# Kernel optimization log

Measured on AMD Instinct MI355X. Metric: run time of the kernel, lower is better.

Reference implementation:

```python
import jax, jax.numpy as jnp
import numpy as np

VOCAB, D_MODEL, HEADS, PAD_ID = 32000, 512, 8, 0
D_K = D_MODEL // HEADS
EPS = 1e-5


def pos_encoding(T, d):
    pos = jnp.arange(T, dtype=jnp.float32)[:, None]              # [T,1]
    freqs = 1.0 / (10000.0 ** (jnp.arange(0, d, 2, dtype=jnp.float32) / d))
    ang = pos * freqs                                            # [T,d/2]
    pe = jnp.zeros((T, d), dtype=jnp.float32)
    pe = pe.at[:, 0::2].set(jnp.sin(ang)).at[:, 1::2].set(jnp.cos(ang))
    return pe


def layer_norm(x, g, b):
    mu = jnp.mean(x, axis=-1, keepdims=True)
    var = jnp.var(x, axis=-1, keepdims=True)
    return (x - mu) * jax.lax.rsqrt(var + EPS) * g + b


def setup_inputs() -> dict:
    key = jax.random.key(0)
    ks = jax.random.split(key, 12)
    B, T = 4, 2048
    s = 0.02
    inp = {
        "tokens": jax.random.randint(ks[0], (B, T), 0, VOCAB),
        "emb": jax.random.normal(ks[1], (VOCAB, D_MODEL), jnp.float32) * s,
        "wq": jax.random.normal(ks[2], (D_MODEL, D_MODEL), jnp.float32) * s,
        "bq": jnp.zeros((D_MODEL,), jnp.float32),
        "wk": jax.random.normal(ks[3], (D_MODEL, D_MODEL), jnp.float32) * s,
        "bk": jnp.zeros((D_MODEL,), jnp.float32),
        "wv": jax.random.normal(ks[4], (D_MODEL, D_MODEL), jnp.float32) * s,
        "bv": jnp.zeros((D_MODEL,), jnp.float32),
        "wo": jax.random.normal(ks[5], (D_MODEL, D_MODEL), jnp.float32) * s,
        "bo": jnp.zeros((D_MODEL,), jnp.float32),
        "w1": jax.random.normal(ks[6], (D_MODEL, 2 * D_MODEL), jnp.float32) * s,
        "b1": jnp.zeros((2 * D_MODEL,), jnp.float32),
        "w2": jax.random.normal(ks[7], (2 * D_MODEL, D_MODEL), jnp.float32) * s,
        "b2": jnp.zeros((D_MODEL,), jnp.float32),
        "ln1_g": jnp.ones((D_MODEL,), jnp.float32),
        "ln1_b": jnp.zeros((D_MODEL,), jnp.float32),
        "ln2_g": jnp.ones((D_MODEL,), jnp.float32),
        "ln2_b": jnp.zeros((D_MODEL,), jnp.float32),
    }
    return inp


def reference(tokens, emb, wq, bq, wk, bk, wv, bv, wo, bo,
              w1, b1, w2, b2, ln1_g, ln1_b, ln2_g, ln2_b):
    B, T = tokens.shape
    x = emb[tokens] * jnp.sqrt(jnp.float32(D_MODEL))             # [B,T,D]
    x = x + pos_encoding(T, D_MODEL)[None]                       # add PE
    q = (x @ wq + bq).reshape(B, T, HEADS, D_K)
    k = (x @ wk + bk).reshape(B, T, HEADS, D_K)
    v = (x @ wv + bv).reshape(B, T, HEADS, D_K)
    scores = jnp.einsum("bqhd,bkhd->bhqk", q, k) / jnp.sqrt(jnp.float32(D_K))
    key_pad_mask = tokens == PAD_ID                              # [B,T]
    neg = jnp.finfo(scores.dtype).min
    scores = jnp.where(key_pad_mask[:, None, None, :], neg, scores)
    attn = jax.nn.softmax(scores, axis=-1)                       # [B,H,T,T]
    av = jnp.einsum("bhqk,bkhd->bqhd", attn, v).reshape(B, T, D_MODEL)
    av = av @ wo + bo
    h = layer_norm(av + x, ln1_g, ln1_b)
    ff = jax.nn.relu(h @ w1 + b1) @ w2 + b2
    out = layer_norm(h + ff, ln2_g, ln2_b)
    return out, key_pad_mask
```

## Files before the change

kernel.cpp:

```cpp
#include <hip/hip_runtime.h>
#include <hip/hip_bf16.h>
#include <math.h>

#define D_MODEL 512
#define HEADS   8
#define D_K     64
#define T_SEQ   2048
#define B_SZ    4
#define NROWS   (B_SZ * T_SEQ)
#define KVB     64
#define KSPLIT  2
#define KHALF   (T_SEQ / KSPLIT)

#define BN 128
#define BKG 64

typedef __attribute__((ext_vector_type(8))) short short8;
typedef __attribute__((ext_vector_type(4))) float f32x4;
typedef __attribute__((ext_vector_type(4))) ushort bf16x4;
typedef __attribute__((ext_vector_type(4))) unsigned int u32x4;

typedef __attribute__((address_space(1))) const unsigned int as1_uint;
typedef __attribute__((address_space(3))) unsigned int as3_uint;

__device__ __forceinline__ ushort f2bf(float f) {
    union { float f; unsigned u; } v; v.f = f;
    unsigned u = v.u;
    unsigned r = (u + 0x7FFFu + ((u >> 16) & 1u)) >> 16;
    return (ushort)r;
}
__device__ __forceinline__ float bf2f(ushort u) {
    union { unsigned u; float f; } v; v.u = ((unsigned)u) << 16;
    return v.f;
}
__device__ __forceinline__ unsigned pk_bf16(float lo, float hi) {
    unsigned r;
    asm("v_cvt_pk_bf16_f32 %0, %1, %2" : "=v"(r) : "v"(lo), "v"(hi));
    return r;
}

__global__ __launch_bounds__(256) void k_prep(
    const int* __restrict__ tokens, const float* __restrict__ emb,
    const float* __restrict__ wq, const float* __restrict__ wk,
    const float* __restrict__ wv, const float* __restrict__ wo,
    const float* __restrict__ w1, const float* __restrict__ w2,
    const float* __restrict__ bq, const float* __restrict__ bk,
    const float* __restrict__ bv,
    ushort* __restrict__ xb, float* __restrict__ mask_out,
    ushort* __restrict__ wqkvT, ushort* __restrict__ woT,
    ushort* __restrict__ w1T, ushort* __restrict__ w2T,
    float* __restrict__ bqkv, float qsc)
{
    __shared__ ushort tls[32][33];
    int bid = blockIdx.x, tid = threadIdx.x;
    if (bid < 4096) {
        int row = bid * 2 + (tid >> 7);
        int t   = row & (T_SEQ - 1);
        int tok = tokens[row];
        int t2  = tid & 127;
        if (t2 == 0) mask_out[row] = (tok == 0) ? 1.0f : 0.0f;
        const float* e = emb + (size_t)tok * D_MODEL;
#pragma unroll
        for (int i = 0; i < 4; ++i) {
            int d = t2 + 128 * i;
            float freq = exp2f(-(float)(d & ~1) * 0.025952563240330564f);
            float sn, cs;
            sincosf((float)t * freq, &sn, &cs);
            float x = e[d] * 22.627416997969522f + ((d & 1) ? cs : sn);
            xb[(size_t)row * D_MODEL + d] = f2bf(x);
        }
        return;
    }
    const float* src; ushort* dst; float scale = 1.0f; int K, N, bx, by;
    if (bid < 5120) {
        int b = bid - 4096; int z = b >> 8; int rem = b & 255;
        bx = rem & 15; by = rem >> 4; K = 512; N = 512;
        src = (z == 0) ? wq : (z == 1) ? wk : (z == 2) ? wv : wo;
        dst = (z < 3) ? wqkvT + (size_t)z * 512 * 512 : woT;
        scale = (z == 0) ? qsc : 1.0f;
    } else if (bid < 5632) {
        int b = bid - 5120; bx = b & 31; by = b >> 5; K = 512; N = 1024; src = w1; dst = w1T;
    } else if (bid < 6144) {
        int b = bid - 5632; bx = b & 15; by = b >> 4; K = 1024; N = 512; src = w2; dst = w2T;
    } else {
        int i = (bid - 6144) * 256 + tid;
        if (i < 512)       bqkv[i] = bq[i] * qsc;
        else if (i < 1024) bqkv[i] = bk[i - 512];
        else if (i < 1536) bqkv[i] = bv[i - 1024];
        return;
    }
    int tx = tid & 31, ty = tid >> 5;
    int n0 = bx * 32, k0 = by * 32;
#pragma unroll
    for (int i = 0; i < 4; ++i)
        tls[ty + i * 8][tx] = f2bf(src[(size_t)(k0 + ty + i * 8) * N + n0 + tx] * scale);
    __syncthreads();
#pragma unroll
    for (int i = 0; i < 4; ++i)
        dst[(size_t)(n0 + ty + i * 8) * K + k0 + tx] = tls[tx][ty + i * 8];
}

__global__ __launch_bounds__(256) void k_rl(const float* __restrict__ lp,
                                            float* __restrict__ rl) {
    int i = blockIdx.x * 256 + threadIdx.x;
    rl[i] = 1.0f / (lp[i] + lp[8 * NROWS + i]);
}

template<int MODE, bool RELU, int BMT, bool COMBA>
__global__ __launch_bounds__(256) void k_gemm_lds(
    const ushort* __restrict__ A, const ushort* __restrict__ A2,
    const float* __restrict__ rlb,
    const ushort* __restrict__ BT,
    const float* __restrict__ bias, void* __restrict__ C0,
    void* __restrict__ C1, void* __restrict__ C2,
    int M, int N, int K)
{
    constexpr int MR = BMT / 32;
    __shared__ __attribute__((aligned(16))) ushort As[2][BMT * BKG];
    __shared__ __attribute__((aligned(16))) ushort Bs[2][BN * BKG];

    const int tid = threadIdx.x;
    const int w = tid >> 6, l = tid & 63;
    const int lr = l & 15, lg = l >> 4;
    const int wr = w >> 1, wc = w & 1;

    int bx = blockIdx.x, by = blockIdx.y;
    {
        int nx = gridDim.x, ny = gridDim.y;
        if ((ny & 7) == 0) {
            int lin = bx + nx * by;
            int xcd = lin & 7, idx = lin >> 3;
            int per = ny >> 3;
            by = xcd * per + (idx % per);
            bx = idx / per;
        }
    }
    const int brow0 = by * BMT;
    const int bcol0 = bx * BN;
    const int swz = lr & 7;

    f32x4 acc[MR][4] = {};
    const int nks = K >> 6;

#define STAGE_B(buf, k0)                                                        \
    {                                                                           \
        _Pragma("unroll")                                                       \
        for (int i = 0; i < 4; ++i) {                                           \
            int gi = w * 256 + i * 64 + l;                                      \
            int row = gi >> 3, slot = gi & 7;                                   \
            int g = slot ^ (row & 7);                                           \
            __builtin_amdgcn_global_load_lds(                                   \
                (as1_uint*)(BT + (size_t)(bcol0 + row) * K + (k0) + g * 8),     \
                (as3_uint*)(&Bs[buf][gi * 8]), 16, 0, 0);                       \
        }                                                                       \
    }
#define STAGE_A_DMA(buf, k0)                                                    \
    {                                                                           \
        _Pragma("unroll")                                                       \
        for (int i = 0; i < BMT / 32; ++i) {                                    \
            int gi = w * (BMT * 2) + i * 64 + l;                                \
            int row = gi >> 3, slot = gi & 7;                                   \
            int g = slot ^ (row & 7);                                           \
            __builtin_amdgcn_global_load_lds(                                   \
                (as1_uint*)(A + (size_t)(brow0 + row) * K + (k0) + g * 8),      \
                (as3_uint*)(&As[buf][gi * 8]), 16, 0, 0);                       \
        }                                                                       \
    }
#define STAGE_A_COMB(buf, k0)                                                   \
    {                                                                           \
        int head = (k0) >> 6;                                                   \
        _Pragma("unroll")                                                       \
        for (int i = 0; i < BMT / 32; ++i) {                                    \
            int gi = w * (BMT * 2) + i * 64 + l;                                \
            int row = gi >> 3, slot = gi & 7;                                   \
            int g = slot ^ (row & 7);                                           \
            size_t off = (size_t)(brow0 + row) * K + (k0) + g * 8;              \
            bf16x4 a0 = *(const bf16x4*)(A + off);                              \
            bf16x4 a1 = *(const bf16x4*)(A + off + 4);                          \
            bf16x4 c0 = *(const bf16x4*)(A2 + off);                             \
            bf16x4 c1 = *(const bf16x4*)(A2 + off + 4);                         \
            float r = rlb[(size_t)head * NROWS + brow0 + row];                  \
            u32x4 pk;                                                           \
            pk[0] = pk_bf16((bf2f(a0[0]) + bf2f(c0[0])) * r,                    \
                            (bf2f(a0[1]) + bf2f(c0[1])) * r);                   \
            pk[1] = pk_bf16((bf2f(a0[2]) + bf2f(c0[2])) * r,                    \
                            (bf2f(a0[3]) + bf2f(c0[3])) * r);                   \
            pk[2] = pk_bf16((bf2f(a1[0]) + bf2f(c1[0])) * r,                    \
                            (bf2f(a1[1]) + bf2f(c1[1])) * r);                   \
            pk[3] = pk_bf16((bf2f(a1[2]) + bf2f(c1[2])) * r,                    \
                            (bf2f(a1[3]) + bf2f(c1[3])) * r);                   \
            *(u32x4*)(&As[buf][gi * 8]) = pk;                                   \
        }                                                                       \
    }
#define STAGE(buf, k0)                                                          \
    {                                                                           \
        if constexpr (COMBA) { STAGE_A_COMB(buf, k0); }                         \
        else                 { STAGE_A_DMA(buf, k0); }                          \
        STAGE_B(buf, k0);                                                       \
    }

    STAGE(0, 0);
    __syncthreads();

    int buf = 0;
    for (int ks = 0; ks < nks; ++ks) {
        if (ks + 1 < nks) STAGE(buf ^ 1, (ks + 1) * BKG);
#pragma unroll
        for (int kk = 0; kk < 2; ++kk) {
            short8 af[MR], bfr[4];
#pragma unroll
            for (int m = 0; m < MR; ++m) {
                int row = wr * (BMT / 2) + m * 16 + lr;
                int slot = (kk * 4 + lg) ^ swz;
                af[m] = *(const short8*)(&As[buf][row * 64 + slot * 8]);
            }
#pragma unroll
            for (int n = 0; n < 4; ++n) {
                int row = wc * 64 + n * 16 + lr;
                int slot = (kk * 4 + lg) ^ swz;
                bfr[n] = *(const short8*)(&Bs[buf][row * 64 + slot * 8]);
            }
#pragma unroll
            for (int m = 0; m < MR; ++m)
#pragma unroll
                for (int n = 0; n < 4; ++n)
                    acc[m][n] = __builtin_amdgcn_mfma_f32_16x16x32_bf16(af[m], bfr[n], acc[m][n], 0, 0, 0);
        }
        __syncthreads();
        buf ^= 1;
    }
#undef STAGE
#undef STAGE_A_COMB
#undef STAGE_A_DMA
#undef STAGE_B

#pragma unroll
    for (int n = 0; n < 4; ++n) {
        int col = bcol0 + wc * 64 + n * 16 + lr;
        float bv = bias[col];
#pragma unroll
        for (int m = 0; m < MR; ++m) {
            int row0 = brow0 + wr * (BMT / 2) + m * 16 + 4 * lg;
            if constexpr (MODE == 2) {
                int seg = col >> 9, lc = col & 511;
                if (seg == 2) {
                    bf16x4 pk;
#pragma unroll
                    for (int j = 0; j < 4; ++j) pk[j] = f2bf(acc[m][n][j] + bv);
                    *(bf16x4*)((ushort*)C2 + (size_t)lc * M + row0) = pk;
                } else {
                    ushort* dst = (seg == 0) ? (ushort*)C0 : (ushort*)C1;
#pragma unroll
                    for (int j = 0; j < 4; ++j)
                        dst[(size_t)(row0 + j) * 512 + lc] = f2bf(acc[m][n][j] + bv);
                }
            } else if constexpr (MODE == 0) {
#pragma unroll
                for (int j = 0; j < 4; ++j) {
                    float v = acc[m][n][j] + bv;
                    if (RELU) v = fmaxf(v, 0.0f);
                    ((ushort*)C0)[(size_t)(row0 + j) * N + col] = f2bf(v);
                }
            } else {
#pragma unroll
                for (int j = 0; j < 4; ++j)
                    ((float*)C0)[(size_t)(row0 + j) * N + col] = acc[m][n][j] + bv;
            }
        }
    }
}

__global__ __launch_bounds__(512, 4) void k_attn(
    const ushort* __restrict__ Q, const ushort* __restrict__ Kb,
    const ushort* __restrict__ Vt, const int* __restrict__ tokens,
    ushort* __restrict__ O0, ushort* __restrict__ O1,
    float* __restrict__ lp)
{
    __shared__ __attribute__((aligned(16))) ushort Kl[2][KVB * 64];
    __shared__ __attribute__((aligned(16))) ushort Vl[2][KVB * 64];
    __shared__ __attribute__((aligned(16))) ushort Mbh[KHALF];
    __shared__ int padf[KHALF / KVB];

    const int tid = threadIdx.x;
    const int w = tid >> 6, l = tid & 63;
    const int lr = l & 15, lg = l >> 4;
    const int swz = lr & 7;

    int lin = blockIdx.x + 8 * (blockIdx.y + 8 * blockIdx.z);
    int xcd = lin & 7, idx = lin >> 3;
    int qt  = idx & 7;
    int grp = xcd + 8 * (idx >> 3);
    int ks  = grp & 1;
    int h   = (grp >> 1) & 7;
    int b   = grp >> 4;

    const int q0  = qt * 256 + w * 32;
    const int kb0 = ks * KHALF;

    const int gi   = w * 64 + l;
    const int srow = gi >> 3;
    const int sg   = gi & 7;
    const int sgx  = sg ^ (srow & 7);
    const ushort* Ksrc = Kb + ((size_t)(b * T_SEQ + kb0) + srow) * D_MODEL + h * D_K + sgx * 8;
    const int kbase = 32 * (sg >> 2) + 8 * ((sg >> 1) & 1) + 4 * (sg & 1);
    const ushort* Vsrc = Vt + (size_t)(h * D_K + srow) * NROWS + b * T_SEQ + kb0 + kbase;
    const int vds = srow * 128 + sgx * 16;

#define KSTAGE(bufi, kt_)                                                       \
    __builtin_amdgcn_global_load_lds(                                           \
        (as1_uint*)(Ksrc + (size_t)(kt_) * KVB * D_MODEL),                      \
        (as3_uint*)(&Kl[bufi][gi * 8]), 16, 0, 0);

    const ushort* Qh = Q + (size_t)b * T_SEQ * D_MODEL + h * D_K;
    short8 aq[2][2];
#pragma unroll
    for (int qs = 0; qs < 2; ++qs)
#pragma unroll
        for (int c2 = 0; c2 < 2; ++c2)
            aq[qs][c2] = *(const short8*)(Qh + (size_t)(q0 + qs * 16 + lr) * D_MODEL
                                          + c2 * 32 + 8 * lg);

    short8 vones;
#pragma unroll
    for (int i = 0; i < 8; ++i) vones[i] = (short)0x3F80;

    const int* tk = tokens + b * T_SEQ + kb0;
#pragma unroll
    for (int it = 0; it < KHALF / 512; ++it) {
        int i = tid + it * 512;
        bool pad = (tk[i] == 0);
        Mbh[i] = pad ? (ushort)0xFF7F : (ushort)0;
        unsigned long long bal = __ballot(pad);
        if (l == 0) padf[it * 8 + w] = (bal != 0ull);
    }

    f32x4 acc[2][4] = {};
    f32x4 acc_l[2] = {};

    {
        bf16x4 va = *(const bf16x4*)(Vsrc);
        bf16x4 vb2 = *(const bf16x4*)(Vsrc + 16);
        KSTAGE(0, 0);
        u32x4 pk = { ((const unsigned*)&va)[0], ((const unsigned*)&va)[1],
                     ((const unsigned*)&vb2)[0], ((const unsigned*)&vb2)[1] };
        *(u32x4*)((char*)Vl[0] + vds) = pk;
    }
    __syncthreads();

    int buf = 0;
    const int NT = KHALF / KVB;
#pragma unroll 2
    for (int kt = 0; kt < NT; ++kt) {
        bf16x4 vna, vnb;
        bool more = (kt + 1 < NT);
        if (more) {
            KSTAGE(buf ^ 1, kt + 1);
            vna = *(const bf16x4*)(Vsrc + (kt + 1) * KVB);
            vnb = *(const bf16x4*)(Vsrc + (kt + 1) * KVB + 16);
        }

        const ushort* Kt = Kl[buf];
        const ushort* Vb = Vl[buf];
        bool havePad = padf[kt];

        unsigned dw[2][4][2];
#pragma unroll
        for (int kh = 0; kh < 2; ++kh) {
            short8 kf[2][2];
#pragma unroll
            for (int i = 0; i < 2; ++i)
#pragma unroll
                for (int c2 = 0; c2 < 2; ++c2)
                    kf[i][c2] = *(const short8*)((const char*)Kt
                                + ((2 * kh + i) * 16 + lr) * 128
                                + (((c2 * 4 + lg) ^ swz) * 16));
#pragma unroll
            for (int qs = 0; qs < 2; ++qs)
#pragma unroll
                for (int i = 0; i < 2; ++i) {
                    int kb = 2 * kh + i;
                    __builtin_amdgcn_s_setprio(1);
                    f32x4 sf = {};
                    sf = __builtin_amdgcn_mfma_f32_16x16x32_bf16(kf[i][0], aq[qs][0], sf, 0, 0, 0);
                    sf = __builtin_amdgcn_mfma_f32_16x16x32_bf16(kf[i][1], aq[qs][1], sf, 0, 0, 0);
                    __builtin_amdgcn_s_setprio(0);
                    if (havePad) {
                        bf16x4 m4 = *(const bf16x4*)(Mbh + kt * KVB + kb * 16 + 4 * lg);
#pragma unroll
                        for (int j = 0; j < 4; ++j) sf[j] += bf2f(m4[j]);
                    }
                    dw[qs][kb][0] = pk_bf16(exp2f(sf[0]), exp2f(sf[1]));
                    dw[qs][kb][1] = pk_bf16(exp2f(sf[2]), exp2f(sf[3]));
                }
        }

#pragma unroll
        for (int ch = 0; ch < 2; ++ch) {
            short8 vf[2][2];
#pragma unroll
            for (int i = 0; i < 2; ++i)
#pragma unroll
                for (int kk = 0; kk < 2; ++kk)
                    vf[i][kk] = *(const short8*)((const char*)Vb
                                + ((2 * ch + i) * 16 + lr) * 128
                                + (((kk * 4 + lg) ^ swz) * 16));
            __builtin_amdgcn_s_setprio(1);
#pragma unroll
            for (int qs = 0; qs < 2; ++qs) {
                u32x4 pw0 = { dw[qs][0][0], dw[qs][0][1], dw[qs][1][0], dw[qs][1][1] };
                u32x4 pw1 = { dw[qs][2][0], dw[qs][2][1], dw[qs][3][0], dw[qs][3][1] };
                short8 pa0 = __builtin_bit_cast(short8, pw0);
                short8 pa1 = __builtin_bit_cast(short8, pw1);
#pragma unroll
                for (int i = 0; i < 2; ++i) {
                    int c = 2 * ch + i;
                    acc[qs][c] = __builtin_amdgcn_mfma_f32_16x16x32_bf16(vf[i][0], pa0, acc[qs][c], 0, 0, 0);
                    acc[qs][c] = __builtin_amdgcn_mfma_f32_16x16x32_bf16(vf[i][1], pa1, acc[qs][c], 0, 0, 0);
                }
                if (ch == 0) {
                    acc_l[qs] = __builtin_amdgcn_mfma_f32_16x16x32_bf16(vones, pa0, acc_l[qs], 0, 0, 0);
                    acc_l[qs] = __builtin_amdgcn_mfma_f32_16x16x32_bf16(vones, pa1, acc_l[qs], 0, 0, 0);
                }
            }
            __builtin_amdgcn_s_setprio(0);
        }

        if (more) {
            u32x4 pk = { ((const unsigned*)&vna)[0], ((const unsigned*)&vna)[1],
                         ((const unsigned*)&vnb)[0], ((const unsigned*)&vnb)[1] };
            *(u32x4*)((char*)Vl[buf ^ 1] + vds) = pk;
        }
        __syncthreads();
        buf ^= 1;
    }
#undef KSTAGE

    ushort* Op = (ks == 0) ? O0 : O1;
#pragma unroll
    for (int qs = 0; qs < 2; ++qs) {
        ushort* orow = Op + (size_t)(b * T_SEQ + q0 + qs * 16 + lr) * D_MODEL + h * D_K;
#pragma unroll
        for (int c = 0; c < 4; ++c) {
            bf16x4 pk;
#pragma unroll
            for (int j = 0; j < 4; ++j) pk[j] = f2bf(acc[qs][c][j]);
            *(bf16x4*)(orow + c * 16 + 4 * lg) = pk;
        }
        if (l < 16)
            lp[(size_t)(ks * 8 + h) * NROWS + b * T_SEQ + q0 + qs * 16 + l] = acc_l[qs][0];
    }
}

template<bool A_BF16, bool RES_BF16, bool OUT_F32>
__global__ __launch_bounds__(256) void k_ln(
    const void* __restrict__ A, const void* __restrict__ Res,
    const float* __restrict__ g, const float* __restrict__ bb,
    float* __restrict__ of, ushort* __restrict__ ob)
{
    int row = blockIdx.x * 4 + (threadIdx.x >> 6);
    int l = threadIdx.x & 63;
    float v[8];
    float s = 0.0f, ss = 0.0f;
#pragma unroll
    for (int i = 0; i < 2; ++i) {
        int d0 = i * 256 + l * 4;
        f32x4 va, vb;
        if (A_BF16) {
            bf16x4 t = *(const bf16x4*)((const ushort*)A + (size_t)row * D_MODEL + d0);
#pragma unroll
            for (int j = 0; j < 4; ++j) va[j] = bf2f(t[j]);
        } else {
            va = *(const f32x4*)((const float*)A + (size_t)row * D_MODEL + d0);
        }
        if (RES_BF16) {
            bf16x4 t = *(const bf16x4*)((const ushort*)Res + (size_t)row * D_MODEL + d0);
#pragma unroll
            for (int j = 0; j < 4; ++j) vb[j] = bf2f(t[j]);
        } else {
            vb = *(const f32x4*)((const float*)Res + (size_t)row * D_MODEL + d0);
        }
#pragma unroll
        for (int j = 0; j < 4; ++j) {
            float x = va[j] + vb[j];
            v[i * 4 + j] = x; s += x; ss += x * x;
        }
    }
#pragma unroll
    for (int d = 1; d < 64; d <<= 1) { s += __shfl_xor(s, d); ss += __shfl_xor(ss, d); }
    float mu  = s * (1.0f / 512.0f);
    float var = ss * (1.0f / 512.0f) - mu * mu;
    float rs  = rsqrtf(var + 1e-5f);
#pragma unroll
    for (int i = 0; i < 2; ++i)
#pragma unroll
        for (int j = 0; j < 4; ++j) {
            int d = i * 256 + l * 4 + j;
            float o = (v[i * 4 + j] - mu) * rs * g[d] + bb[d];
            if (OUT_F32) of[(size_t)row * D_MODEL + d] = o;
            else         ob[(size_t)row * D_MODEL + d] = f2bf(o);
        }
}

extern "C" void kernel_launch(void* const* d_in, const int* in_sizes, int n_in,
                              void* d_out, int out_size, void* d_ws, size_t ws_size,
                              hipStream_t stream)
{
    const int*   tokens = (const int*)  d_in[0];
    const float* emb    = (const float*)d_in[1];
    const float* wq     = (const float*)d_in[2];
    const float* bq     = (const float*)d_in[3];
    const float* wk     = (const float*)d_in[4];
    const float* bk     = (const float*)d_in[5];
    const float* wv     = (const float*)d_in[6];
    const float* bv     = (const float*)d_in[7];
    const float* wo     = (const float*)d_in[8];
    const float* bo     = (const float*)d_in[9];
    const float* w1     = (const float*)d_in[10];
    const float* b1     = (const float*)d_in[11];
    const float* w2     = (const float*)d_in[12];
    const float* b2     = (const float*)d_in[13];
    const float* ln1_g  = (const float*)d_in[14];
    const float* ln1_b  = (const float*)d_in[15];
    const float* ln2_g  = (const float*)d_in[16];
    const float* ln2_b  = (const float*)d_in[17];

    char* ws = (char*)d_ws;
    ushort* xb   = (ushort*)(ws + 0);
    ushort* Qb   = (ushort*)(ws + 8388608);
    ushort* Kbuf = (ushort*)(ws + 16777216);
    ushort* Vt   = (ushort*)(ws + 25165824);
    ushort* atb  = (ushort*)(ws + 33554432);
    ushort* AVb  = (ushort*)(ws + 41943040);
    ushort* wqkvT = (ushort*)(ws + 50331648);
    ushort* woT  = wqkvT + 1536 * 512;
    ushort* w1T  = woT + 262144;
    ushort* w2T  = w1T + 524288;
    float*  bqkv = (float*)(w2T + 524288);
    float*  lpart = bqkv + 2048;
    float*  rlbuf = lpart + 2 * 8 * NROWS;
    float*  WOf   = (float*)(rlbuf + 8 * NROWS);

    ushort* hb   = Qb;
    ushort* ff1b = Kbuf;
    ushort* ff2b = AVb;
    ushort* wob  = AVb;
    (void)WOf;

    float* out_f    = (float*)d_out;
    float* mask_out = out_f + (size_t)NROWS * D_MODEL;

    const float QSC = 0.18033688011112042f;

    k_prep<<<6150, 256, 0, stream>>>(
        tokens, emb, wq, wk, wv, wo, w1, w2, bq, bk, bv,
        xb, mask_out, wqkvT, woT, w1T, w2T, bqkv, QSC);

    k_gemm_lds<2, false, 128, false><<<dim3(12, 64), 256, 0, stream>>>(
        xb, nullptr, nullptr, wqkvT, bqkv, Qb, Kbuf, Vt, NROWS, 1536, 512);

    k_attn<<<dim3(8, 8, 8), 512, 0, stream>>>(
        Qb, Kbuf, Vt, tokens, atb, AVb, lpart);
    k_rl<<<8 * NROWS / 256, 256, 0, stream>>>(lpart, rlbuf);

    k_gemm_lds<0, false, 64, true><<<dim3(4, 128), 256, 0, stream>>>(
        atb, AVb, rlbuf, woT, bo, Qb, nullptr, nullptr, NROWS, 512, 512);

    k_ln<true, true, false><<<NROWS / 4, 256, 0, stream>>>(
        Qb, xb, ln1_g, ln1_b, nullptr, atb);

    k_gemm_lds<0, true, 64, false><<<dim3(8, 128), 256, 0, stream>>>(
        atb, nullptr, nullptr, w1T, b1, ff1b, nullptr, nullptr, NROWS, 1024, 512);
    k_gemm_lds<0, false, 64, false><<<dim3(4, 128), 256, 0, stream>>>(
        ff1b, nullptr, nullptr, w2T, b2, ff2b, nullptr, nullptr, NROWS, 512, 1024);

    k_ln<true, true, true><<<NROWS / 4, 256, 0, stream>>>(
        ff2b, atb, ln2_g, ln2_b, out_f, nullptr);
}
```

Before: 150.4 us.

## Give each attention wave 64 query rows with 256-thread blocks

```diff
diff --git a/kernel.cpp b/kernel.cpp
--- a/kernel.cpp
+++ b/kernel.cpp
@@ -65,7 +65,7 @@
             int d = t2 + 128 * i;
             float freq = exp2f(-(float)(d & ~1) * 0.025952563240330564f);
             float sn, cs;
-            sincosf((float)t * freq, &sn, &cs);
+            __sincosf((float)t * freq, &sn, &cs);
             float x = e[d] * 22.627416997969522f + ((d & 1) ? cs : sn);
             xb[(size_t)row * D_MODEL + d] = f2bf(x);
         }
@@ -270,7 +270,7 @@
     }
 }
 
-__global__ __launch_bounds__(512, 4) void k_attn(
+__global__ __launch_bounds__(256, 2) void k_attn(
     const ushort* __restrict__ Q, const ushort* __restrict__ Kb,
     const ushort* __restrict__ Vt, const int* __restrict__ tokens,
     ushort* __restrict__ O0, ushort* __restrict__ O1,
@@ -294,27 +294,36 @@
     int h   = (grp >> 1) & 7;
     int b   = grp >> 4;
 
-    const int q0  = qt * 256 + w * 32;
+    const int q0  = qt * 256 + w * 64;
     const int kb0 = ks * KHALF;
 
-    const int gi   = w * 64 + l;
-    const int srow = gi >> 3;
-    const int sg   = gi & 7;
-    const int sgx  = sg ^ (srow & 7);
-    const ushort* Ksrc = Kb + ((size_t)(b * T_SEQ + kb0) + srow) * D_MODEL + h * D_K + sgx * 8;
-    const int kbase = 32 * (sg >> 2) + 8 * ((sg >> 1) & 1) + 4 * (sg & 1);
-    const ushort* Vsrc = Vt + (size_t)(h * D_K + srow) * NROWS + b * T_SEQ + kb0 + kbase;
-    const int vds = srow * 128 + sgx * 16;
+    const int row0s = tid >> 3,        sg0 = tid & 7;
+    const int row1s = (tid + 256) >> 3, sg1 = (tid + 256) & 7;
+    const int sgx0 = sg0 ^ (row0s & 7);
+    const int sgx1 = sg1 ^ (row1s & 7);
+    const ushort* Ksrc0 = Kb + ((size_t)(b * T_SEQ + kb0) + row0s) * D_MODEL + h * D_K + sgx0 * 8;
+    const ushort* Ksrc1 = Kb + ((size_t)(b * T_SEQ + kb0) + row1s) * D_MODEL + h * D_K + sgx1 * 8;
+    const int kbase0 = 32 * (sg0 >> 2) + 8 * ((sg0 >> 1) & 1) + 4 * (sg0 & 1);
+    const int kbase1 = 32 * (sg1 >> 2) + 8 * ((sg1 >> 1) & 1) + 4 * (sg1 & 1);
+    const ushort* Vsrc0 = Vt + (size_t)(h * D_K + row0s) * NROWS + b * T_SEQ + kb0 + kbase0;
+    const ushort* Vsrc1 = Vt + (size_t)(h * D_K + row1s) * NROWS + b * T_SEQ + kb0 + kbase1;
+    const int vds0 = row0s * 128 + sgx0 * 16;
+    const int vds1 = row1s * 128 + sgx1 * 16;
 
 #define KSTAGE(bufi, kt_)                                                       \
-    __builtin_amdgcn_global_load_lds(                                           \
-        (as1_uint*)(Ksrc + (size_t)(kt_) * KVB * D_MODEL),                      \
-        (as3_uint*)(&Kl[bufi][gi * 8]), 16, 0, 0);
+    {                                                                           \
+        __builtin_amdgcn_global_load_lds(                                       \
+            (as1_uint*)(Ksrc0 + (size_t)(kt_) * KVB * D_MODEL),                 \
+            (as3_uint*)(&Kl[bufi][tid * 8]), 16, 0, 0);                         \
+        __builtin_amdgcn_global_load_lds(                                       \
+            (as1_uint*)(Ksrc1 + (size_t)(kt_) * KVB * D_MODEL),                 \
+            (as3_uint*)(&Kl[bufi][(tid + 256) * 8]), 16, 0, 0);                 \
+    }
 
     const ushort* Qh = Q + (size_t)b * T_SEQ * D_MODEL + h * D_K;
-    short8 aq[2][2];
-#pragma unroll
-    for (int qs = 0; qs < 2; ++qs)
+    short8 aq[4][2];
+#pragma unroll
+    for (int qs = 0; qs < 4; ++qs)
 #pragma unroll
         for (int c2 = 0; c2 < 2; ++c2)
             aq[qs][c2] = *(const short8*)(Qh + (size_t)(q0 + qs * 16 + lr) * D_MODEL
@@ -326,44 +335,50 @@
 
     const int* tk = tokens + b * T_SEQ + kb0;
 #pragma unroll
-    for (int it = 0; it < KHALF / 512; ++it) {
-        int i = tid + it * 512;
+    for (int it = 0; it < KHALF / 256; ++it) {
+        int i = tid + it * 256;
         bool pad = (tk[i] == 0);
         Mbh[i] = pad ? (ushort)0xFF7F : (ushort)0;
         unsigned long long bal = __ballot(pad);
-        if (l == 0) padf[it * 8 + w] = (bal != 0ull);
-    }
-
-    f32x4 acc[2][4] = {};
-    f32x4 acc_l[2] = {};
+        if (l == 0) padf[it * 4 + w] = (bal != 0ull);
+    }
+
+    f32x4 acc[4][4] = {};
+    f32x4 acc_l[4] = {};
 
     {
-        bf16x4 va = *(const bf16x4*)(Vsrc);
-        bf16x4 vb2 = *(const bf16x4*)(Vsrc + 16);
+        bf16x4 va0 = *(const bf16x4*)(Vsrc0);
+        bf16x4 vb0 = *(const bf16x4*)(Vsrc0 + 16);
+        bf16x4 va1 = *(const bf16x4*)(Vsrc1);
+        bf16x4 vb1 = *(const bf16x4*)(Vsrc1 + 16);
         KSTAGE(0, 0);
-        u32x4 pk = { ((const unsigned*)&va)[0], ((const unsigned*)&va)[1],
-                     ((const unsigned*)&vb2)[0], ((const unsigned*)&vb2)[1] };
-        *(u32x4*)((char*)Vl[0] + vds) = pk;
+        u32x4 p0 = { ((const unsigned*)&va0)[0], ((const unsigned*)&va0)[1],
+                     ((const unsigned*)&vb0)[0], ((const unsigned*)&vb0)[1] };
+        u32x4 p1 = { ((const unsigned*)&va1)[0], ((const unsigned*)&va1)[1],
+                     ((const unsigned*)&vb1)[0], ((const unsigned*)&vb1)[1] };
+        *(u32x4*)((char*)Vl[0] + vds0) = p0;
+        *(u32x4*)((char*)Vl[0] + vds1) = p1;
     }
     __syncthreads();
 
     int buf = 0;
     const int NT = KHALF / KVB;
-#pragma unroll 2
     for (int kt = 0; kt < NT; ++kt) {
-        bf16x4 vna, vnb;
+        bf16x4 vna0, vnb0, vna1, vnb1;
         bool more = (kt + 1 < NT);
         if (more) {
             KSTAGE(buf ^ 1, kt + 1);
-            vna = *(const bf16x4*)(Vsrc + (kt + 1) * KVB);
-            vnb = *(const bf16x4*)(Vsrc + (kt + 1) * KVB + 16);
+            vna0 = *(const bf16x4*)(Vsrc0 + (kt + 1) * KVB);
+            vnb0 = *(const bf16x4*)(Vsrc0 + (kt + 1) * KVB + 16);
+            vna1 = *(const bf16x4*)(Vsrc1 + (kt + 1) * KVB);
+            vnb1 = *(const bf16x4*)(Vsrc1 + (kt + 1) * KVB + 16);
         }
 
         const ushort* Kt = Kl[buf];
         const ushort* Vb = Vl[buf];
         bool havePad = padf[kt];
 
-        unsigned dw[2][4][2];
+        unsigned dw[4][4][2];
 #pragma unroll
         for (int kh = 0; kh < 2; ++kh) {
             short8 kf[2][2];
@@ -375,7 +390,7 @@
                                 + ((2 * kh + i) * 16 + lr) * 128
                                 + (((c2 * 4 + lg) ^ swz) * 16));
 #pragma unroll
-            for (int qs = 0; qs < 2; ++qs)
+            for (int qs = 0; qs < 4; ++qs)
 #pragma unroll
                 for (int i = 0; i < 2; ++i) {
                     int kb = 2 * kh + i;
@@ -406,7 +421,7 @@
                                 + (((kk * 4 + lg) ^ swz) * 16));
             __builtin_amdgcn_s_setprio(1);
 #pragma unroll
-            for (int qs = 0; qs < 2; ++qs) {
+            for (int qs = 0; qs < 4; ++qs) {
                 u32x4 pw0 = { dw[qs][0][0], dw[qs][0][1], dw[qs][1][0], dw[qs][1][1] };
                 u32x4 pw1 = { dw[qs][2][0], dw[qs][2][1], dw[qs][3][0], dw[qs][3][1] };
                 short8 pa0 = __builtin_bit_cast(short8, pw0);
@@ -426,9 +441,12 @@
         }
 
         if (more) {
-            u32x4 pk = { ((const unsigned*)&vna)[0], ((const unsigned*)&vna)[1],
-                         ((const unsigned*)&vnb)[0], ((const unsigned*)&vnb)[1] };
-            *(u32x4*)((char*)Vl[buf ^ 1] + vds) = pk;
+            u32x4 p0 = { ((const unsigned*)&vna0)[0], ((const unsigned*)&vna0)[1],
+                         ((const unsigned*)&vnb0)[0], ((const unsigned*)&vnb0)[1] };
+            u32x4 p1 = { ((const unsigned*)&vna1)[0], ((const unsigned*)&vna1)[1],
+                         ((const unsigned*)&vnb1)[0], ((const unsigned*)&vnb1)[1] };
+            *(u32x4*)((char*)Vl[buf ^ 1] + vds0) = p0;
+            *(u32x4*)((char*)Vl[buf ^ 1] + vds1) = p1;
         }
         __syncthreads();
         buf ^= 1;
@@ -437,7 +455,7 @@
 
     ushort* Op = (ks == 0) ? O0 : O1;
 #pragma unroll
-    for (int qs = 0; qs < 2; ++qs) {
+    for (int qs = 0; qs < 4; ++qs) {
         ushort* orow = Op + (size_t)(b * T_SEQ + q0 + qs * 16 + lr) * D_MODEL + h * D_K;
 #pragma unroll
         for (int c = 0; c < 4; ++c) {
@@ -538,13 +556,9 @@
     float*  bqkv = (float*)(w2T + 524288);
     float*  lpart = bqkv + 2048;
     float*  rlbuf = lpart + 2 * 8 * NROWS;
-    float*  WOf   = (float*)(rlbuf + 8 * NROWS);
-
-    ushort* hb   = Qb;
+
     ushort* ff1b = Kbuf;
     ushort* ff2b = AVb;
-    ushort* wob  = AVb;
-    (void)WOf;
 
     float* out_f    = (float*)d_out;
     float* mask_out = out_f + (size_t)NROWS * D_MODEL;
@@ -558,7 +572,7 @@
     k_gemm_lds<2, false, 128, false><<<dim3(12, 64), 256, 0, stream>>>(
         xb, nullptr, nullptr, wqkvT, bqkv, Qb, Kbuf, Vt, NROWS, 1536, 512);
 
-    k_attn<<<dim3(8, 8, 8), 512, 0, stream>>>(
+    k_attn<<<dim3(8, 8, 8), 256, 0, stream>>>(
         Qb, Kbuf, Vt, tokens, atb, AVb, lpart);
     k_rl<<<8 * NROWS / 256, 256, 0, stream>>>(lpart, rlbuf);
 
```

After: 155.6 us. 3.5% more time.
